# Kernel tuning notes

Measured on AMD Instinct MI355X. Metric: run time of the kernel, lower is better.

The kernel has to match this reference:

```python
import jax, jax.numpy as jnp
import numpy as np


def setup_inputs() -> dict:
    key = jax.random.key(0)
    k1, k2 = jax.random.split(key)
    B, N, C = 2, 1024, 64  # batch_size, block_num, out_channels
    regional_means = jax.random.normal(k1, (B, N, C), dtype=jnp.float32)
    # nn.Parameter randn then kaiming_uniform_: just use scaled random weights
    W = jax.random.normal(k2, (C, C), dtype=jnp.float32) * (1.0 / np.sqrt(C))
    return {"regional_means": regional_means, "W": W, "c": C}


def reference(regional_means, W, c):
    # regional_means: (B, N, c); W: (c, c)
    B, N, _ = regional_means.shape
    M = W @ W.T  # (c, c), PSD Mahalanobis metric
    # pairwise differences diff[b, i, j] = means[b, i] - means[b, j]  -> (B, N, N, c)
    # (original materializes this via repeat/permute; sign flip from its final
    #  permute is irrelevant since the quadratic form is even)
    diff = regional_means[:, :, None, :] - regional_means[:, None, :, :]
    # quadratic form q[b,i,j] = diff^T M diff
    q = jnp.einsum('bijc,cd,bijd->bij', diff, M, diff)
    adj = jnp.exp(-q) + jnp.eye(N, dtype=regional_means.dtype)[None, :, :]
    return adj
```

## Files before the change

### kernel.cpp

```cpp
#include <hip/hip_runtime.h>
#include <hip/hip_bf16.h>
#include <math.h>


typedef __attribute__((ext_vector_type(8))) short bf16x8;
typedef __attribute__((ext_vector_type(4))) float f32x4;

#define PITCH 72

static __device__ __forceinline__ void store4bf(__hip_bfloat16* p, float4 v) {
    __hip_bfloat16 h[4] = {__float2bfloat16(v.x), __float2bfloat16(v.y),
                           __float2bfloat16(v.z), __float2bfloat16(v.w)};
    *(uint2*)p = *(const uint2*)h;
}

__global__ void __launch_bounds__(256, 2) adj_fused_mfma(
    const float* __restrict__ X, const float* __restrict__ W,
    float* __restrict__ out, int N)
{
    __shared__ __hip_bfloat16 sXi[64][PITCH];
    __shared__ __hip_bfloat16 sXj[64][PITCH];
    __shared__ __hip_bfloat16 sWT[64][PITCH];
    __shared__ __hip_bfloat16 sYi[64][PITCH];
    __shared__ __hip_bfloat16 sYj[64][PITCH];
    __shared__ float rs[2][64];

    const int b    = blockIdx.z;
    const int ib   = blockIdx.y << 6;
    const int jb   = blockIdx.x << 6;
    const bool diag = (ib == jb);
    const int t    = threadIdx.x;
    const int wave = t >> 6;
    const int lane = t & 63;
    const int m    = lane & 15;
    const int q    = lane >> 4;
    const int r16  = wave << 4;

    const float* __restrict__ Xb = X + (size_t)b * N * 64;

    const float4* W4  = (const float4*)W;
    const float4* Xi4 = (const float4*)(Xb + (size_t)ib * 64);
    const float4* Xj4 = (const float4*)(Xb + (size_t)jb * 64);
#pragma unroll
    for (int it = 0; it < 4; ++it) {
        const int idx = it * 256 + t;
        const int row = idx >> 4;
        const int c4  = (idx & 15) << 2;
        const float4 wv = W4[idx];
        sWT[c4 + 0][row] = __float2bfloat16(wv.x);
        sWT[c4 + 1][row] = __float2bfloat16(wv.y);
        sWT[c4 + 2][row] = __float2bfloat16(wv.z);
        sWT[c4 + 3][row] = __float2bfloat16(wv.w);
        store4bf(&sXi[row][c4], Xi4[idx]);
        if (!diag) store4bf(&sXj[row][c4], Xj4[idx]);
    }
    __syncthreads();

    auto computeY = [&](const __hip_bfloat16 (*sX)[PITCH],
                        __hip_bfloat16 (*sY)[PITCH], float* rdst) {
        const bf16x8 a0 = *(const bf16x8*)&sX[r16 + m][q * 8];
        const bf16x8 a1 = *(const bf16x8*)&sX[r16 + m][q * 8 + 32];
        float p[4] = {0.f, 0.f, 0.f, 0.f};
#pragma unroll
        for (int ci = 0; ci < 4; ++ci) {
            const bf16x8 b0 = *(const bf16x8*)&sWT[(ci << 4) + m][q * 8];
            const bf16x8 b1 = *(const bf16x8*)&sWT[(ci << 4) + m][q * 8 + 32];
            f32x4 acc = {0.f, 0.f, 0.f, 0.f};
            acc = __builtin_amdgcn_mfma_f32_16x16x32_bf16(a0, b0, acc, 0, 0, 0);
            acc = __builtin_amdgcn_mfma_f32_16x16x32_bf16(a1, b1, acc, 0, 0, 0);
#pragma unroll
            for (int v = 0; v < 4; ++v) {
                const __hip_bfloat16 hb = __float2bfloat16(acc[v]);
                sY[r16 + q * 4 + v][(ci << 4) + m] = hb;
                const float f = __bfloat162float(hb);
                p[v] = fmaf(f, f, p[v]);
            }
        }
#pragma unroll
        for (int off = 1; off < 16; off <<= 1)
#pragma unroll
            for (int v = 0; v < 4; ++v) p[v] += __shfl_xor(p[v], off, 64);
        if (m == 0)
#pragma unroll
            for (int v = 0; v < 4; ++v) rdst[r16 + q * 4 + v] = p[v];
    };

    computeY(sXi, sYi, rs[0]);
    if (!diag) computeY(sXj, sYj, rs[1]);
    __syncthreads();

    const __hip_bfloat16 (*pYj)[PITCH] = diag ? sYi : sYj;
    const float* prj = diag ? rs[0] : rs[1];

    const bf16x8 ga0 = *(const bf16x8*)&sYi[r16 + m][q * 8];
    const bf16x8 ga1 = *(const bf16x8*)&sYi[r16 + m][q * 8 + 32];

    const size_t obase = (size_t)b * N * N;
    float ri[4];
#pragma unroll
    for (int v = 0; v < 4; ++v) ri[v] = rs[0][r16 + q * 4 + v];

#pragma unroll
    for (int mj = 0; mj < 4; ++mj) {
        const bf16x8 gb0 = *(const bf16x8*)&pYj[(mj << 4) + m][q * 8];
        const bf16x8 gb1 = *(const bf16x8*)&pYj[(mj << 4) + m][q * 8 + 32];
        f32x4 acc = {0.f, 0.f, 0.f, 0.f};
        acc = __builtin_amdgcn_mfma_f32_16x16x32_bf16(ga0, gb0, acc, 0, 0, 0);
        acc = __builtin_amdgcn_mfma_f32_16x16x32_bf16(ga1, gb1, acc, 0, 0, 0);
        const int gj = jb + (mj << 4) + m;
        const float rjv = prj[(mj << 4) + m];
#pragma unroll
        for (int v = 0; v < 4; ++v) {
            const int gi = ib + r16 + q * 4 + v;
            const float qq = ri[v] + rjv - 2.f * acc[v];
            float val = __expf(-qq);
            if (gi == gj) val += 1.f;
            out[obase + (size_t)gi * N + gj] = val;
        }
    }
}

extern "C" void kernel_launch(void* const* d_in, const int* in_sizes, int n_in,
                              void* d_out, int out_size, void* d_ws, size_t ws_size,
                              hipStream_t stream) {
    (void)n_in; (void)d_ws; (void)ws_size;
    const float* X = (const float*)d_in[0];
    const float* W = (const float*)d_in[1];
    float* out = (float*)d_out;

    const int C  = 64;
    const int BN = in_sizes[0] / C;
    const int N  = (int)(((long long)out_size * C) / in_sizes[0]);
    const int B  = BN / N;

    adj_fused_mfma<<<dim3(N / 64, N / 64, B), 256, 0, stream>>>(X, W, out, N);
}
```

Baseline: 63.77 us.

## Vectorize output stores via transposed MFMA and use 512-thread blocks

The final MFMA swaps its operands so each lane holds four consecutive j outputs, which allows one 16-byte float4 store in place of four scalar stores. The block grows to 8 waves: the Y=XW projections for the i and j tiles run in parallel across wave groups, and the output tile is split between j-bands and i-halves. Y is written in place over the bf16 X tiles, which cuts LDS use and may allow more resident blocks. The in-place write relies on each wave reading its own rows before overwriting them.

Result: no change. 63.26 us (median of 2 runs) (-0.8%).

```diff
diff --git a/kernel.cpp b/kernel.cpp
--- a/kernel.cpp
+++ b/kernel.cpp
@@ -14,15 +14,12 @@
     *(uint2*)p = *(const uint2*)h;
 }
 
-__global__ void __launch_bounds__(256, 2) adj_fused_mfma(
+__global__ void __launch_bounds__(512, 4) adj_fused_mfma2(
     const float* __restrict__ X, const float* __restrict__ W,
     float* __restrict__ out, int N)
 {
-    __shared__ __hip_bfloat16 sXi[64][PITCH];
-    __shared__ __hip_bfloat16 sXj[64][PITCH];
+    __shared__ __hip_bfloat16 sX[2][64][PITCH];
     __shared__ __hip_bfloat16 sWT[64][PITCH];
-    __shared__ __hip_bfloat16 sYi[64][PITCH];
-    __shared__ __hip_bfloat16 sYj[64][PITCH];
     __shared__ float rs[2][64];
 
     const int b    = blockIdx.z;
@@ -30,11 +27,10 @@
     const int jb   = blockIdx.x << 6;
     const bool diag = (ib == jb);
     const int t    = threadIdx.x;
-    const int wave = t >> 6;
+    const int w    = t >> 6;
     const int lane = t & 63;
     const int m    = lane & 15;
     const int q    = lane >> 4;
-    const int r16  = wave << 4;
 
     const float* __restrict__ Xb = X + (size_t)b * N * 64;
 
@@ -42,8 +38,8 @@
     const float4* Xi4 = (const float4*)(Xb + (size_t)ib * 64);
     const float4* Xj4 = (const float4*)(Xb + (size_t)jb * 64);
 #pragma unroll
-    for (int it = 0; it < 4; ++it) {
-        const int idx = it * 256 + t;
+    for (int it = 0; it < 2; ++it) {
+        const int idx = it * 512 + t;
         const int row = idx >> 4;
         const int c4  = (idx & 15) << 2;
         const float4 wv = W4[idx];
@@ -51,72 +47,78 @@
         sWT[c4 + 1][row] = __float2bfloat16(wv.y);
         sWT[c4 + 2][row] = __float2bfloat16(wv.z);
         sWT[c4 + 3][row] = __float2bfloat16(wv.w);
-        store4bf(&sXi[row][c4], Xi4[idx]);
-        if (!diag) store4bf(&sXj[row][c4], Xj4[idx]);
+        store4bf(&sX[0][row][c4], Xi4[idx]);
+        if (!diag) store4bf(&sX[1][row][c4], Xj4[idx]);
     }
     __syncthreads();
 
-    auto computeY = [&](const __hip_bfloat16 (*sX)[PITCH],
-                        __hip_bfloat16 (*sY)[PITCH], float* rdst) {
-        const bf16x8 a0 = *(const bf16x8*)&sX[r16 + m][q * 8];
-        const bf16x8 a1 = *(const bf16x8*)&sX[r16 + m][q * 8 + 32];
-        float p[4] = {0.f, 0.f, 0.f, 0.f};
+    {
+        const int src  = w >> 2;
+        const int band = (w & 3) << 4;
+        if (!(diag && src)) {
+            const bf16x8 a0 = *(const bf16x8*)&sX[src][band + m][q * 8];
+            const bf16x8 a1 = *(const bf16x8*)&sX[src][band + m][q * 8 + 32];
+            float p[4] = {0.f, 0.f, 0.f, 0.f};
 #pragma unroll
-        for (int ci = 0; ci < 4; ++ci) {
-            const bf16x8 b0 = *(const bf16x8*)&sWT[(ci << 4) + m][q * 8];
-            const bf16x8 b1 = *(const bf16x8*)&sWT[(ci << 4) + m][q * 8 + 32];
-            f32x4 acc = {0.f, 0.f, 0.f, 0.f};
-            acc = __builtin_amdgcn_mfma_f32_16x16x32_bf16(a0, b0, acc, 0, 0, 0);
-            acc = __builtin_amdgcn_mfma_f32_16x16x32_bf16(a1, b1, acc, 0, 0, 0);
+            for (int ci = 0; ci < 4; ++ci) {
+                const bf16x8 b0 = *(const bf16x8*)&sWT[(ci << 4) + m][q * 8];
+                const bf16x8 b1 = *(const bf16x8*)&sWT[(ci << 4) + m][q * 8 + 32];
+                f32x4 acc = {0.f, 0.f, 0.f, 0.f};
+                acc = __builtin_amdgcn_mfma_f32_16x16x32_bf16(a0, b0, acc, 0, 0, 0);
+                acc = __builtin_amdgcn_mfma_f32_16x16x32_bf16(a1, b1, acc, 0, 0, 0);
 #pragma unroll
-            for (int v = 0; v < 4; ++v) {
-                const __hip_bfloat16 hb = __float2bfloat16(acc[v]);
-                sY[r16 + q * 4 + v][(ci << 4) + m] = hb;
-                const float f = __bfloat162float(hb);
-                p[v] = fmaf(f, f, p[v]);
+                for (int v = 0; v < 4; ++v) {
+                    const __hip_bfloat16 hb = __float2bfloat16(acc[v]);
+                    sX[src][band + q * 4 + v][(ci << 4) + m] = hb;
+                    const float f = __bfloat162float(hb);
+                    p[v] = fmaf(f, f, p[v]);
+                }
             }
+#pragma unroll
+            for (int off = 1; off < 16; off <<= 1)
+#pragma unroll
+                for (int v = 0; v < 4; ++v) p[v] += __shfl_xor(p[v], off, 64);
+            if (m == 0)
+#pragma unroll
+                for (int v = 0; v < 4; ++v) rs[src][band + q * 4 + v] = p[v];
         }
-#pragma unroll
-        for (int off = 1; off < 16; off <<= 1)
-#pragma unroll
-            for (int v = 0; v < 4; ++v) p[v] += __shfl_xor(p[v], off, 64);
-        if (m == 0)
-#pragma unroll
-            for (int v = 0; v < 4; ++v) rdst[r16 + q * 4 + v] = p[v];
-    };
-
-    computeY(sXi, sYi, rs[0]);
-    if (!diag) computeY(sXj, sYj, rs[1]);
+    }
     __syncthreads();
 
-    const __hip_bfloat16 (*pYj)[PITCH] = diag ? sYi : sYj;
+    const __hip_bfloat16 (*pYi)[PITCH] = sX[0];
+    const __hip_bfloat16 (*pYj)[PITCH] = diag ? sX[0] : sX[1];
     const float* prj = diag ? rs[0] : rs[1];
 
-    const bf16x8 ga0 = *(const bf16x8*)&sYi[r16 + m][q * 8];
-    const bf16x8 ga1 = *(const bf16x8*)&sYi[r16 + m][q * 8 + 32];
+    const int jband = (w & 3) << 4;
+    const int ihalf = w >> 2;
+
+    const bf16x8 ja0 = *(const bf16x8*)&pYj[jband + m][q * 8];
+    const bf16x8 ja1 = *(const bf16x8*)&pYj[jband + m][q * 8 + 32];
+    float rj[4];
+#pragma unroll
+    for (int v = 0; v < 4; ++v) rj[v] = prj[jband + (q << 2) + v];
 
     const size_t obase = (size_t)b * N * N;
-    float ri[4];
 #pragma unroll
-    for (int v = 0; v < 4; ++v) ri[v] = rs[0][r16 + q * 4 + v];
-
-#pragma unroll
-    for (int mj = 0; mj < 4; ++mj) {
-        const bf16x8 gb0 = *(const bf16x8*)&pYj[(mj << 4) + m][q * 8];
-        const bf16x8 gb1 = *(const bf16x8*)&pYj[(mj << 4) + m][q * 8 + 32];
+    for (int s = 0; s < 2; ++s) {
+        const int isub   = (ihalf << 1) + s;
+        const int ilocal = (isub << 4) + m;
+        const bf16x8 ib0 = *(const bf16x8*)&pYi[ilocal][q * 8];
+        const bf16x8 ib1 = *(const bf16x8*)&pYi[ilocal][q * 8 + 32];
         f32x4 acc = {0.f, 0.f, 0.f, 0.f};
-        acc = __builtin_amdgcn_mfma_f32_16x16x32_bf16(ga0, gb0, acc, 0, 0, 0);
-        acc = __builtin_amdgcn_mfma_f32_16x16x32_bf16(ga1, gb1, acc, 0, 0, 0);
-        const int gj = jb + (mj << 4) + m;
-        const float rjv = prj[(mj << 4) + m];
+        acc = __builtin_amdgcn_mfma_f32_16x16x32_bf16(ja0, ib0, acc, 0, 0, 0);
+        acc = __builtin_amdgcn_mfma_f32_16x16x32_bf16(ja1, ib1, acc, 0, 0, 0);
+        const float riv = rs[0][ilocal];
+        f32x4 vals;
 #pragma unroll
         for (int v = 0; v < 4; ++v) {
-            const int gi = ib + r16 + q * 4 + v;
-            const float qq = ri[v] + rjv - 2.f * acc[v];
+            const float qq = riv + rj[v] - 2.f * acc[v];
             float val = __expf(-qq);
-            if (gi == gj) val += 1.f;
-            out[obase + (size_t)gi * N + gj] = val;
+            if (diag && ilocal == jband + (q << 2) + v) val += 1.f;
+            vals[v] = val;
         }
+        *(f32x4*)&out[obase + (size_t)(ib + ilocal) * N + jb + jband + (q << 2)]
+            = vals;
     }
 }
 
@@ -133,5 +135,5 @@
     const int N  = (int)(((long long)out_size * C) / in_sizes[0]);
     const int B  = BN / N;
 
-    adj_fused_mfma<<<dim3(N / 64, N / 64, B), 256, 0, stream>>>(X, W, out, N);
+    adj_fused_mfma2<<<dim3(N / 64, N / 64, B), 512, 0, stream>>>(X, W, out, N);
 }
```
